# Kernel optimization log

Measured on AMD Instinct MI355X. Metric: run time of the kernel, lower is better.

## Reference

```python
import jax, jax.numpy as jnp
import numpy as np
from jax import lax

B, T, D, L = 64, 512, 1024, 32


def setup_inputs() -> dict:
    key = jax.random.key(0)
    k = jax.random.split(key, 8)
    x = jax.random.normal(k[0], (B, T, D), dtype=jnp.float32)
    mask = jnp.ones((B, T), dtype=bool)
    labels = jax.random.randint(k[1], (B, T), 0, L)
    W = jax.random.normal(k[2], (D, L), dtype=jnp.float32) / np.sqrt(D)
    b = jnp.zeros((L,), dtype=jnp.float32)
    transitions = jax.random.normal(k[3], (L, L), dtype=jnp.float32) * 0.1
    start_transitions = jax.random.normal(k[4], (L,), dtype=jnp.float32) * 0.1
    end_transitions = jax.random.normal(k[5], (L,), dtype=jnp.float32) * 0.1
    return {"x": x, "mask": mask, "labels": labels, "W": W, "b": b,
            "transitions": transitions, "start_transitions": start_transitions,
            "end_transitions": end_transitions}


def _log_partition(logits, mask, transitions, start_t, end_t):
    # logits: [B,T,L], mask: [B,T] bool. AllenNLP _input_likelihood.
    alpha0 = start_t[None, :] + logits[:, 0]  # [B,L]
    logits_t = jnp.swapaxes(logits, 0, 1)[1:]  # [T-1,B,L]
    mask_t = jnp.swapaxes(mask, 0, 1)[1:]      # [T-1,B]

    def step(alpha, inp):
        logit, m = inp  # [B,L], [B]
        # inner[b,i,j] = alpha[b,i] + transitions[i,j] + logit[b,j]
        inner = alpha[:, :, None] + transitions[None, :, :] + logit[:, None, :]
        new = jax.nn.logsumexp(inner, axis=1)
        return jnp.where(m[:, None], new, alpha), None

    alpha, _ = lax.scan(step, alpha0, (logits_t, mask_t))
    return jax.nn.logsumexp(alpha + end_t[None, :], axis=-1)  # [B]


def _joint_score(logits, tags, mask, transitions, start_t, end_t):
    # AllenNLP _joint_likelihood, vectorized over time.
    maskf = mask.astype(logits.dtype)
    score = start_t[tags[:, 0]]
    trans = transitions[tags[:, :-1], tags[:, 1:]]  # [B,T-1]
    score = score + jnp.sum(trans * maskf[:, 1:], axis=1)
    emit = jnp.take_along_axis(logits[:, :-1], tags[:, :-1, None], axis=2)[..., 0]
    score = score + jnp.sum(emit * maskf[:, :-1], axis=1)
    lengths = jnp.sum(mask.astype(jnp.int32), axis=1)
    last_tags = jnp.take_along_axis(tags, (lengths - 1)[:, None], axis=1)[:, 0]
    score = score + end_t[last_tags]
    last_emit = jnp.take_along_axis(logits[:, -1], last_tags[:, None], axis=1)[:, 0]
    score = score + last_emit * maskf[:, -1]
    return score  # [B]


def reference(x, mask, labels, W, b, transitions, start_transitions, end_transitions):
    logits = jnp.einsum('btd,dl->btl', x, W) + b  # Linear classifier
    probabilities = jax.nn.softmax(logits, axis=-1)
    logZ = _log_partition(logits, mask, transitions, start_transitions, end_transitions)
    gold = _joint_score(logits, labels, mask, transitions, start_transitions, end_transitions)
    log_likelihood = jnp.sum(gold - logZ)
    loss = -log_likelihood
    return probabilities, loss
```

## Files before the change

kernel.cpp:

```cpp
#include <hip/hip_runtime.h>

#define OUT_LOSS_IDX 1048576

typedef __attribute__((ext_vector_type(4)))  float f32x4;
typedef __attribute__((ext_vector_type(16))) float f32x16;
typedef __attribute__((ext_vector_type(4)))  int i32x4;
typedef __attribute__((ext_vector_type(4)))  unsigned u32x4;
typedef __attribute__((ext_vector_type(8)))  short bf16x8;

__device__ __forceinline__ unsigned short f32_to_bf16(float f) {
    unsigned u = __float_as_uint(f);
    unsigned r = (u + 0x7FFFu + ((u >> 16) & 1u)) >> 16;
    return (unsigned short)r;
}
__device__ __forceinline__ unsigned packbf(float lo, float hi) {
    return __builtin_amdgcn_perm(__float_as_uint(hi) + 0x8000u,
                                 __float_as_uint(lo) + 0x8000u, 0x07060302u);
}

__global__ void k0_wt(const float* __restrict__ W, unsigned short* __restrict__ Wt,
                      float* __restrict__ loss) {
    int idx = blockIdx.x * 256 + threadIdx.x;
    int k = idx >> 5, c = idx & 31;
    Wt[c * 1024 + k] = f32_to_bf16(W[idx]);
    if (idx == 0) loss[0] = 0.f;
}

__global__ __launch_bounds__(64) void k1_gemm(
    const float* __restrict__ x, const unsigned short* __restrict__ Wt,
    const float* __restrict__ bias, float* __restrict__ logits,
    float* __restrict__ probs) {
    const int lane = threadIdx.x;
    const int m = lane & 15, quad = lane >> 4;
    const int r0 = blockIdx.x * 16;

    const float* xa = x + (size_t)(r0 + m) * 1024 + quad * 8;
    const unsigned short* wb0 = Wt + (size_t)m * 1024 + quad * 8;
    const unsigned short* wb1 = Wt + (size_t)(m + 16) * 1024 + quad * 8;

    f32x4 acc0 = {0.f, 0.f, 0.f, 0.f};
    f32x4 acc1 = {0.f, 0.f, 0.f, 0.f};

    #pragma unroll 4
    for (int ks = 0; ks < 32; ++ks) {
        f32x4 a0 = *(const f32x4*)(xa + ks * 32);
        f32x4 a1 = *(const f32x4*)(xa + ks * 32 + 4);
        bf16x8 b0 = *(const bf16x8*)(wb0 + ks * 32);
        bf16x8 b1 = *(const bf16x8*)(wb1 + ks * 32);
        bf16x8 af;
        af[0] = (short)f32_to_bf16(a0[0]); af[1] = (short)f32_to_bf16(a0[1]);
        af[2] = (short)f32_to_bf16(a0[2]); af[3] = (short)f32_to_bf16(a0[3]);
        af[4] = (short)f32_to_bf16(a1[0]); af[5] = (short)f32_to_bf16(a1[1]);
        af[6] = (short)f32_to_bf16(a1[2]); af[7] = (short)f32_to_bf16(a1[3]);
        acc0 = __builtin_amdgcn_mfma_f32_16x16x32_bf16(af, b0, acc0, 0, 0, 0);
        acc1 = __builtin_amdgcn_mfma_f32_16x16x32_bf16(af, b1, acc1, 0, 0, 0);
    }
    const float bc0 = bias[m], bc1 = bias[16 + m];
    #pragma unroll
    for (int r = 0; r < 4; ++r) {
        int row = r0 + quad * 4 + r;
        float l0 = acc0[r] + bc0;
        float l1 = acc1[r] + bc1;
        logits[row * 32 + m] = l0;
        logits[row * 32 + 16 + m] = l1;
        float mx = fmaxf(l0, l1);
        #pragma unroll
        for (int d = 1; d < 16; d <<= 1) mx = fmaxf(mx, __shfl_xor(mx, d, 64));
        float e0 = __expf(l0 - mx), e1 = __expf(l1 - mx);
        float s = e0 + e1;
        #pragma unroll
        for (int d = 1; d < 16; d <<= 1) s += __shfl_xor(s, d, 64);
        float inv = 1.0f / s;
        probs[row * 32 + m] = e0 * inv;
        probs[row * 32 + 16 + m] = e1 * inv;
    }
}

__global__ __launch_bounds__(256, 1) void k3a_chunks(
    const float* __restrict__ logits, const int* __restrict__ mask,
    const float* __restrict__ trans, float* __restrict__ Gws,
    float* __restrict__ chunkLog) {
    __shared__ float sElt[128 * 32];
    __shared__ int smaskL[128];

    const int tid = threadIdx.x;
    const int b = blockIdx.x >> 2, a = blockIdx.x & 3;
    const int w = tid >> 6, lane = tid & 63;
    const int h = lane >> 5, col = lane & 31;

    const float* src = logits + (size_t)b * 16384 + (128 * a + 1) * 32;
    #pragma unroll
    for (int q = 0; q < 4; ++q) {
        int slot = q * 256 + tid;
        f32x4 v = *(const f32x4*)&src[slot * 4];
        f32x4 e = {__expf(v[0]), __expf(v[1]), __expf(v[2]), __expf(v[3])};
        *(f32x4*)&sElt[slot * 4] = e;
    }
    if (tid < 128) {
        int t = 128 * a + 1 + tid;
        smaskL[tid] = (t < 512) ? mask[b * 512 + t] : 0;
    }
    __syncthreads();

    bf16x8 a1, a2;
    #pragma unroll
    for (int j = 0; j < 8; ++j) {
        a1[j] = (short)f32_to_bf16(__expf(trans[(8 * h + j) * 32 + col]));
        a2[j] = (short)f32_to_bf16(__expf(trans[(16 + 8 * h + j) * 32 + col]));
    }

    float c[16];
    #pragma unroll
    for (int r = 0; r < 16; ++r)
        c[r] = (((r & 3) + 8 * (r >> 2) + 4 * h) == col) ? 1.f : 0.f;
    int esum = 0;

    for (int tl = 0; tl < 32; ++tl) {
        const int tt = 32 * w + tl;
        unsigned d0 = packbf(c[0],  c[1]),  d1 = packbf(c[2],  c[3]);
        unsigned d2 = packbf(c[4],  c[5]),  d3 = packbf(c[6],  c[7]);
        unsigned d4 = packbf(c[8],  c[9]),  d5 = packbf(c[10], c[11]);
        unsigned d6 = packbf(c[12], c[13]), d7 = packbf(c[14], c[15]);
        unsigned x0 = (unsigned)__shfl_xor((int)d0, 32, 64);
        unsigned x1 = (unsigned)__shfl_xor((int)d1, 32, 64);
        unsigned x2 = (unsigned)__shfl_xor((int)d2, 32, 64);
        unsigned x3 = (unsigned)__shfl_xor((int)d3, 32, 64);
        unsigned x4 = (unsigned)__shfl_xor((int)d4, 32, 64);
        unsigned x5 = (unsigned)__shfl_xor((int)d5, 32, 64);
        unsigned x6 = (unsigned)__shfl_xor((int)d6, 32, 64);
        unsigned x7 = (unsigned)__shfl_xor((int)d7, 32, 64);
        u32x4 b0w = {h ? x2 : d0, h ? x3 : d1, h ? d2 : x0, h ? d3 : x1};
        u32x4 b1w = {h ? x6 : d4, h ? x7 : d5, h ? d6 : x4, h ? d7 : x5};
        bf16x8 b0 = __builtin_bit_cast(bf16x8, b0w);
        bf16x8 b1 = __builtin_bit_cast(bf16x8, b1w);

        f32x16 zz = {};
        f32x16 acc = __builtin_amdgcn_mfma_f32_32x32x16_bf16(a1, b0, zz, 0, 0, 0);
        acc = __builtin_amdgcn_mfma_f32_32x32x16_bf16(a2, b1, acc, 0, 0, 0);

        const f32x4* ep = (const f32x4*)&sElt[tt * 32];
        f32x4 e0 = ep[h], e1 = ep[2 + h], e2 = ep[4 + h], e3 = ep[6 + h];
        const int mk = smaskL[tt];

        int sb = __builtin_amdgcn_readfirstlane(__float_as_int(c[0]));
        int ee = ((sb >> 23) & 0xff) - 127;
        ee = ee < -60 ? -60 : (ee > 60 ? 60 : ee);
        float sc = __int_as_float((127 - ee) << 23);
        esum += ee;

        #pragma unroll
        for (int r = 0; r < 16; ++r) {
            float ev = (r < 4 ? e0[r & 3] : r < 8 ? e1[r & 3] : r < 12 ? e2[r & 3] : e3[r & 3]);
            float qn = acc[r] * (ev * sc);
            float qa = c[r] * sc;
            c[r] = mk ? qn : qa;
        }
    }

    const int cc = 4 * a + w;
    float* gw = Gws + (((size_t)(b * 16 + cc)) << 10);
    #pragma unroll
    for (int r = 0; r < 16; ++r)
        gw[((r & 3) + 8 * (r >> 2) + 4 * h) * 32 + col] = c[r];
    if (lane == 0)
        chunkLog[b * 16 + cc] = (float)esum * 0.6931471805599453f;
}

__global__ __launch_bounds__(64, 1) void k3b_combine(
    const float* __restrict__ logits, const int* __restrict__ mask,
    const int* __restrict__ labels, const float* __restrict__ trans,
    const float* __restrict__ start_t, const float* __restrict__ end_t,
    const float* __restrict__ Gws, const float* __restrict__ chunkLog,
    float* __restrict__ loss_out) {
    __shared__ __align__(16) float pbuf[2][32];
    __shared__ int smaskL[512];

    const int b = blockIdx.x, lane = threadIdx.x;
    const int j = lane & 31;
    const int base = b * 512;

    #pragma unroll
    for (int it = 0; it < 2; ++it) {
        int idx = it * 64 + lane;
        *(i32x4*)&smaskL[idx * 4] = *(const i32x4*)&mask[base + idx * 4];
    }
    float p = __expf(start_t[j] + logits[(size_t)b * 16384 + j]);
    float logC = 0.f;
    pbuf[0][j] = p;
    __syncthreads();

    for (int cc = 0; cc < 16; ++cc) {
        const float* g = Gws + ((((size_t)(b * 16 + cc)) << 10) + j * 32);
        f32x4 g0 = *(const f32x4*)&g[0],  g1 = *(const f32x4*)&g[4];
        f32x4 g2 = *(const f32x4*)&g[8],  g3 = *(const f32x4*)&g[12];
        f32x4 g4 = *(const f32x4*)&g[16], g5 = *(const f32x4*)&g[20];
        f32x4 g6 = *(const f32x4*)&g[24], g7 = *(const f32x4*)&g[28];
        const float* pb = pbuf[cc & 1];
        f32x4 p0 = *(const f32x4*)&pb[0],  p1 = *(const f32x4*)&pb[4];
        f32x4 p2 = *(const f32x4*)&pb[8],  p3 = *(const f32x4*)&pb[12];
        f32x4 p4 = *(const f32x4*)&pb[16], p5 = *(const f32x4*)&pb[20];
        f32x4 p6 = *(const f32x4*)&pb[24], p7 = *(const f32x4*)&pb[28];
        float r0 = p0[0];
        float s0 = 0.f, s1 = 0.f, s2 = 0.f, s3 = 0.f;
        s0 = fmaf(p0[0], g0[0], s0); s1 = fmaf(p0[1], g0[1], s1);
        s2 = fmaf(p0[2], g0[2], s2); s3 = fmaf(p0[3], g0[3], s3);
        s0 = fmaf(p1[0], g1[0], s0); s1 = fmaf(p1[1], g1[1], s1);
        s2 = fmaf(p1[2], g1[2], s2); s3 = fmaf(p1[3], g1[3], s3);
        s0 = fmaf(p2[0], g2[0], s0); s1 = fmaf(p2[1], g2[1], s1);
        s2 = fmaf(p2[2], g2[2], s2); s3 = fmaf(p2[3], g2[3], s3);
        s0 = fmaf(p3[0], g3[0], s0); s1 = fmaf(p3[1], g3[1], s1);
        s2 = fmaf(p3[2], g3[2], s2); s3 = fmaf(p3[3], g3[3], s3);
        s0 = fmaf(p4[0], g4[0], s0); s1 = fmaf(p4[1], g4[1], s1);
        s2 = fmaf(p4[2], g4[2], s2); s3 = fmaf(p4[3], g4[3], s3);
        s0 = fmaf(p5[0], g5[0], s0); s1 = fmaf(p5[1], g5[1], s1);
        s2 = fmaf(p5[2], g5[2], s2); s3 = fmaf(p5[3], g5[3], s3);
        s0 = fmaf(p6[0], g6[0], s0); s1 = fmaf(p6[1], g6[1], s1);
        s2 = fmaf(p6[2], g6[2], s2); s3 = fmaf(p6[3], g6[3], s3);
        s0 = fmaf(p7[0], g7[0], s0); s1 = fmaf(p7[1], g7[1], s1);
        s2 = fmaf(p7[2], g7[2], s2); s3 = fmaf(p7[3], g7[3], s3);
        float s = (s0 + s1) + (s2 + s3);
        p = s * __builtin_amdgcn_rcpf(r0);
        pbuf[(cc + 1) & 1][j] = p;
        logC += __logf(r0);
    }
    float clsum = 0.f;
    #pragma unroll
    for (int cc = 0; cc < 16; ++cc) clsum += chunkLog[b * 16 + cc];

    float f = logC + clsum + __logf(p) + end_t[j];
    float mx = f;
    #pragma unroll
    for (int d = 1; d < 32; d <<= 1) mx = fmaxf(mx, __shfl_xor(mx, d, 64));
    float e = __expf(f - mx), se = e;
    #pragma unroll
    for (int d = 1; d < 32; d <<= 1) se += __shfl_xor(se, d, 64);
    float logZb = mx + __logf(se);

    const int t0 = lane * 8;
    const int* lb = labels + base + t0;
    i32x4 la = *(const i32x4*)&lb[0];
    i32x4 lc = *(const i32x4*)&lb[4];
    int tg[8] = {la[0], la[1], la[2], la[3], lc[0], lc[1], lc[2], lc[3]};
    int prev = (lane == 0) ? 0 : labels[base + t0 - 1];
    float part = 0.f;
    int cnt = 0;
    #pragma unroll
    for (int r = 0; r < 8; ++r) {
        int t = t0 + r;
        int mk = smaskL[t];
        float mf = mk ? 1.f : 0.f;
        cnt += mk ? 1 : 0;
        int tag = tg[r];
        if (t > 0) part += trans[prev * 32 + tag] * mf;
        if (t < 511) part += logits[(size_t)b * 16384 + t * 32 + tag] * mf;
        prev = tag;
    }
    #pragma unroll
    for (int d = 1; d < 64; d <<= 1) {
        part += __shfl_xor(part, d, 64);
        cnt += __shfl_xor(cnt, d, 64);
    }
    if (lane == 0) {
        int len = cnt;
        int first = labels[base];
        int last = labels[base + len - 1];
        float g = part + start_t[first] + end_t[last];
        g += logits[(size_t)b * 16384 + 511 * 32 + last] * (smaskL[511] ? 1.f : 0.f);
        atomicAdd(loss_out, logZb - g);
    }
}

extern "C" void kernel_launch(void* const* d_in, const int* in_sizes, int n_in,
                              void* d_out, int out_size, void* d_ws, size_t ws_size,
                              hipStream_t stream) {
    const float* x       = (const float*)d_in[0];
    const int* mk        = (const int*)d_in[1];
    const int* labels    = (const int*)d_in[2];
    const float* W       = (const float*)d_in[3];
    const float* bias    = (const float*)d_in[4];
    const float* trans   = (const float*)d_in[5];
    const float* start_t = (const float*)d_in[6];
    const float* end_t   = (const float*)d_in[7];

    float* probs = (float*)d_out;
    float* loss  = probs + OUT_LOSS_IDX;
    float* ws = (float*)d_ws;
    float* logits = ws;
    unsigned short* Wt = (unsigned short*)(ws + 1048576);
    float* Gws = ws + 1048576 + 16384;
    float* chunkLog = Gws + 1048576;

    k0_wt<<<128, 256, 0, stream>>>(W, Wt, loss);
    k1_gemm<<<2048, 64, 0, stream>>>(x, Wt, bias, logits, probs);
    k3a_chunks<<<256, 256, 0, stream>>>(logits, mk, trans, Gws, chunkLog);
    k3b_combine<<<64, 64, 0, stream>>>(logits, mk, labels, trans, start_t, end_t,
                                       Gws, chunkLog, loss);
}
```

Baseline: 239.4 us.

## Split GEMM K across waves, interleave two CRF sub-chains, prefetch combine loads

The logits GEMM now runs four waves per block, each covering a quarter of K, and reduces their partial sums through shared memory, which raises parallelism and memory-level concurrency. Each k3a wave now advances two independent 16-step sub-chains in interleaved fashion to hide MFMA dependency latency, then joins them with one extra matrix product. k3b prefetches the next chunk's transfer matrix while the current one is applied. The costs are extra shared-memory traffic and a barrier in the GEMM, plus one extra bf16 rounding when composing the sub-chain products.

```diff
diff --git a/kernel.cpp b/kernel.cpp
--- a/kernel.cpp
+++ b/kernel.cpp
@@ -16,6 +16,45 @@
 __device__ __forceinline__ unsigned packbf(float lo, float hi) {
     return __builtin_amdgcn_perm(__float_as_uint(hi) + 0x8000u,
                                  __float_as_uint(lo) + 0x8000u, 0x07060302u);
+}
+__device__ __forceinline__ void make_bfrags(const float* c, int h, bf16x8& b0, bf16x8& b1) {
+    unsigned d0 = packbf(c[0],  c[1]),  d1 = packbf(c[2],  c[3]);
+    unsigned d2 = packbf(c[4],  c[5]),  d3 = packbf(c[6],  c[7]);
+    unsigned d4 = packbf(c[8],  c[9]),  d5 = packbf(c[10], c[11]);
+    unsigned d6 = packbf(c[12], c[13]), d7 = packbf(c[14], c[15]);
+    unsigned x0 = (unsigned)__shfl_xor((int)d0, 32, 64);
+    unsigned x1 = (unsigned)__shfl_xor((int)d1, 32, 64);
+    unsigned x2 = (unsigned)__shfl_xor((int)d2, 32, 64);
+    unsigned x3 = (unsigned)__shfl_xor((int)d3, 32, 64);
+    unsigned x4 = (unsigned)__shfl_xor((int)d4, 32, 64);
+    unsigned x5 = (unsigned)__shfl_xor((int)d5, 32, 64);
+    unsigned x6 = (unsigned)__shfl_xor((int)d6, 32, 64);
+    unsigned x7 = (unsigned)__shfl_xor((int)d7, 32, 64);
+    u32x4 b0w = {h ? x2 : d0, h ? x3 : d1, h ? d2 : x0, h ? d3 : x1};
+    u32x4 b1w = {h ? x6 : d4, h ? x7 : d5, h ? d6 : x4, h ? d7 : x5};
+    b0 = __builtin_bit_cast(bf16x8, b0w);
+    b1 = __builtin_bit_cast(bf16x8, b1w);
+}
+__device__ __forceinline__ void crf_step(float* c, const f32x4* ep, int h, int mk,
+                                         bf16x8 a1, bf16x8 a2, int& esum) {
+    bf16x8 b0, b1;
+    make_bfrags(c, h, b0, b1);
+    f32x16 zz = {};
+    f32x16 acc = __builtin_amdgcn_mfma_f32_32x32x16_bf16(a1, b0, zz, 0, 0, 0);
+    acc = __builtin_amdgcn_mfma_f32_32x32x16_bf16(a2, b1, acc, 0, 0, 0);
+    f32x4 e0 = ep[h], e1 = ep[2 + h], e2 = ep[4 + h], e3 = ep[6 + h];
+    int sb = __builtin_amdgcn_readfirstlane(__float_as_int(c[0]));
+    int ee = ((sb >> 23) & 0xff) - 127;
+    ee = ee < -60 ? -60 : (ee > 60 ? 60 : ee);
+    float sc = __int_as_float((127 - ee) << 23);
+    esum += ee;
+    #pragma unroll
+    for (int r = 0; r < 16; ++r) {
+        float ev = (r < 4 ? e0[r & 3] : r < 8 ? e1[r & 3] : r < 12 ? e2[r & 3] : e3[r & 3]);
+        float qn = acc[r] * (ev * sc);
+        float qa = c[r] * sc;
+        c[r] = mk ? qn : qa;
+    }
 }
 
 __global__ void k0_wt(const float* __restrict__ W, unsigned short* __restrict__ Wt,
@@ -26,23 +65,25 @@
     if (idx == 0) loss[0] = 0.f;
 }
 
-__global__ __launch_bounds__(64) void k1_gemm(
+__global__ __launch_bounds__(256) void k1_gemm(
     const float* __restrict__ x, const unsigned short* __restrict__ Wt,
     const float* __restrict__ bias, float* __restrict__ logits,
     float* __restrict__ probs) {
-    const int lane = threadIdx.x;
+    __shared__ float sacc[3][64][9];
+    const int tid = threadIdx.x;
+    const int wv = tid >> 6, lane = tid & 63;
     const int m = lane & 15, quad = lane >> 4;
     const int r0 = blockIdx.x * 16;
 
-    const float* xa = x + (size_t)(r0 + m) * 1024 + quad * 8;
-    const unsigned short* wb0 = Wt + (size_t)m * 1024 + quad * 8;
-    const unsigned short* wb1 = Wt + (size_t)(m + 16) * 1024 + quad * 8;
+    const float* xa = x + (size_t)(r0 + m) * 1024 + wv * 256 + quad * 8;
+    const unsigned short* wb0 = Wt + (size_t)m * 1024 + wv * 256 + quad * 8;
+    const unsigned short* wb1 = Wt + (size_t)(m + 16) * 1024 + wv * 256 + quad * 8;
 
     f32x4 acc0 = {0.f, 0.f, 0.f, 0.f};
     f32x4 acc1 = {0.f, 0.f, 0.f, 0.f};
 
-    #pragma unroll 4
-    for (int ks = 0; ks < 32; ++ks) {
+    #pragma unroll
+    for (int ks = 0; ks < 8; ++ks) {
         f32x4 a0 = *(const f32x4*)(xa + ks * 32);
         f32x4 a1 = *(const f32x4*)(xa + ks * 32 + 4);
         bf16x8 b0 = *(const bf16x8*)(wb0 + ks * 32);
@@ -55,24 +96,39 @@
         acc0 = __builtin_amdgcn_mfma_f32_16x16x32_bf16(af, b0, acc0, 0, 0, 0);
         acc1 = __builtin_amdgcn_mfma_f32_16x16x32_bf16(af, b1, acc1, 0, 0, 0);
     }
-    const float bc0 = bias[m], bc1 = bias[16 + m];
-    #pragma unroll
-    for (int r = 0; r < 4; ++r) {
-        int row = r0 + quad * 4 + r;
-        float l0 = acc0[r] + bc0;
-        float l1 = acc1[r] + bc1;
-        logits[row * 32 + m] = l0;
-        logits[row * 32 + 16 + m] = l1;
-        float mx = fmaxf(l0, l1);
+    if (wv) {
         #pragma unroll
-        for (int d = 1; d < 16; d <<= 1) mx = fmaxf(mx, __shfl_xor(mx, d, 64));
-        float e0 = __expf(l0 - mx), e1 = __expf(l1 - mx);
-        float s = e0 + e1;
+        for (int r = 0; r < 4; ++r) {
+            sacc[wv - 1][lane][r] = acc0[r];
+            sacc[wv - 1][lane][4 + r] = acc1[r];
+        }
+    }
+    __syncthreads();
+    if (wv == 0) {
         #pragma unroll
-        for (int d = 1; d < 16; d <<= 1) s += __shfl_xor(s, d, 64);
-        float inv = 1.0f / s;
-        probs[row * 32 + m] = e0 * inv;
-        probs[row * 32 + 16 + m] = e1 * inv;
+        for (int r = 0; r < 4; ++r) {
+            acc0[r] += sacc[0][lane][r] + sacc[1][lane][r] + sacc[2][lane][r];
+            acc1[r] += sacc[0][lane][4 + r] + sacc[1][lane][4 + r] + sacc[2][lane][4 + r];
+        }
+        const float bc0 = bias[m], bc1 = bias[16 + m];
+        #pragma unroll
+        for (int r = 0; r < 4; ++r) {
+            int row = r0 + quad * 4 + r;
+            float l0 = acc0[r] + bc0;
+            float l1 = acc1[r] + bc1;
+            logits[row * 32 + m] = l0;
+            logits[row * 32 + 16 + m] = l1;
+            float mx = fmaxf(l0, l1);
+            #pragma unroll
+            for (int d = 1; d < 16; d <<= 1) mx = fmaxf(mx, __shfl_xor(mx, d, 64));
+            float e0 = __expf(l0 - mx), e1 = __expf(l1 - mx);
+            float s = e0 + e1;
+            #pragma unroll
+            for (int d = 1; d < 16; d <<= 1) s += __shfl_xor(s, d, 64);
+            float inv = 1.0f / s;
+            probs[row * 32 + m] = e0 * inv;
+            probs[row * 32 + 16 + m] = e1 * inv;
+        }
     }
 }
 
@@ -82,6 +138,7 @@
     float* __restrict__ chunkLog) {
     __shared__ float sElt[128 * 32];
     __shared__ int smaskL[128];
+    __shared__ float qb[4][32][33];
 
     const int tid = threadIdx.x;
     const int b = blockIdx.x >> 2, a = blockIdx.x & 3;
@@ -109,61 +166,49 @@
         a2[j] = (short)f32_to_bf16(__expf(trans[(16 + 8 * h + j) * 32 + col]));
     }
 
-    float c[16];
+    float cA[16], cB[16];
+    #pragma unroll
+    for (int r = 0; r < 16; ++r) {
+        float iv = (((r & 3) + 8 * (r >> 2) + 4 * h) == col) ? 1.f : 0.f;
+        cA[r] = iv; cB[r] = iv;
+    }
+    int esA = 0, esB = 0;
+
+    for (int tl = 0; tl < 16; ++tl) {
+        const int ttA = 32 * w + tl;
+        const int ttB = 32 * w + 16 + tl;
+        crf_step(cA, (const f32x4*)&sElt[ttA * 32], h, smaskL[ttA], a1, a2, esA);
+        crf_step(cB, (const f32x4*)&sElt[ttB * 32], h, smaskL[ttB], a1, a2, esB);
+    }
+
     #pragma unroll
     for (int r = 0; r < 16; ++r)
-        c[r] = (((r & 3) + 8 * (r >> 2) + 4 * h) == col) ? 1.f : 0.f;
-    int esum = 0;
-
-    for (int tl = 0; tl < 32; ++tl) {
-        const int tt = 32 * w + tl;
-        unsigned d0 = packbf(c[0],  c[1]),  d1 = packbf(c[2],  c[3]);
-        unsigned d2 = packbf(c[4],  c[5]),  d3 = packbf(c[6],  c[7]);
-        unsigned d4 = packbf(c[8],  c[9]),  d5 = packbf(c[10], c[11]);
-        unsigned d6 = packbf(c[12], c[13]), d7 = packbf(c[14], c[15]);
-        unsigned x0 = (unsigned)__shfl_xor((int)d0, 32, 64);
-        unsigned x1 = (unsigned)__shfl_xor((int)d1, 32, 64);
-        unsigned x2 = (unsigned)__shfl_xor((int)d2, 32, 64);
-        unsigned x3 = (unsigned)__shfl_xor((int)d3, 32, 64);
-        unsigned x4 = (unsigned)__shfl_xor((int)d4, 32, 64);
-        unsigned x5 = (unsigned)__shfl_xor((int)d5, 32, 64);
-        unsigned x6 = (unsigned)__shfl_xor((int)d6, 32, 64);
-        unsigned x7 = (unsigned)__shfl_xor((int)d7, 32, 64);
-        u32x4 b0w = {h ? x2 : d0, h ? x3 : d1, h ? d2 : x0, h ? d3 : x1};
-        u32x4 b1w = {h ? x6 : d4, h ? x7 : d5, h ? d6 : x4, h ? d7 : x5};
-        bf16x8 b0 = __builtin_bit_cast(bf16x8, b0w);
-        bf16x8 b1 = __builtin_bit_cast(bf16x8, b1w);
-
-        f32x16 zz = {};
-        f32x16 acc = __builtin_amdgcn_mfma_f32_32x32x16_bf16(a1, b0, zz, 0, 0, 0);
-        acc = __builtin_amdgcn_mfma_f32_32x32x16_bf16(a2, b1, acc, 0, 0, 0);
-
-        const f32x4* ep = (const f32x4*)&sElt[tt * 32];
-        f32x4 e0 = ep[h], e1 = ep[2 + h], e2 = ep[4 + h], e3 = ep[6 + h];
-        const int mk = smaskL[tt];
-
-        int sb = __builtin_amdgcn_readfirstlane(__float_as_int(c[0]));
-        int ee = ((sb >> 23) & 0xff) - 127;
-        ee = ee < -60 ? -60 : (ee > 60 ? 60 : ee);
-        float sc = __int_as_float((127 - ee) << 23);
-        esum += ee;
-
-        #pragma unroll
-        for (int r = 0; r < 16; ++r) {
-            float ev = (r < 4 ? e0[r & 3] : r < 8 ? e1[r & 3] : r < 12 ? e2[r & 3] : e3[r & 3]);
-            float qn = acc[r] * (ev * sc);
-            float qa = c[r] * sc;
-            c[r] = mk ? qn : qa;
-        }
-    }
+        qb[w][(r & 3) + 8 * (r >> 2) + 4 * h][col] = cB[r];
+    __syncthreads();
+    bf16x8 aP1, aP2;
+    #pragma unroll
+    for (int j = 0; j < 8; ++j) {
+        aP1[j] = (short)f32_to_bf16(qb[w][col][8 * h + j]);
+        aP2[j] = (short)f32_to_bf16(qb[w][col][16 + 8 * h + j]);
+    }
+    bf16x8 b0, b1;
+    make_bfrags(cA, h, b0, b1);
+    f32x16 zz = {};
+    f32x16 P = __builtin_amdgcn_mfma_f32_32x32x16_bf16(aP1, b0, zz, 0, 0, 0);
+    P = __builtin_amdgcn_mfma_f32_32x32x16_bf16(aP2, b1, P, 0, 0, 0);
+
+    int sb = __builtin_amdgcn_readfirstlane(__float_as_int(P[0]));
+    int ee = ((sb >> 23) & 0xff) - 127;
+    ee = ee < -60 ? -60 : (ee > 60 ? 60 : ee);
+    float sc = __int_as_float((127 - ee) << 23);
 
     const int cc = 4 * a + w;
     float* gw = Gws + (((size_t)(b * 16 + cc)) << 10);
     #pragma unroll
     for (int r = 0; r < 16; ++r)
-        gw[((r & 3) + 8 * (r >> 2) + 4 * h) * 32 + col] = c[r];
+        gw[((r & 3) + 8 * (r >> 2) + 4 * h) * 32 + col] = P[r] * sc;
     if (lane == 0)
-        chunkLog[b * 16 + cc] = (float)esum * 0.6931471805599453f;
+        chunkLog[b * 16 + cc] = (float)(esA + esB + ee) * 0.6931471805599453f;
 }
 
 __global__ __launch_bounds__(64, 1) void k3b_combine(
@@ -184,17 +229,26 @@
         int idx = it * 64 + lane;
         *(i32x4*)&smaskL[idx * 4] = *(const i32x4*)&mask[base + idx * 4];
     }
+    const float* gbase = Gws + (((size_t)(b * 16)) << 10) + j * 32;
+    f32x4 g0 = *(const f32x4*)&gbase[0],  g1 = *(const f32x4*)&gbase[4];
+    f32x4 g2 = *(const f32x4*)&gbase[8],  g3 = *(const f32x4*)&gbase[12];
+    f32x4 g4 = *(const f32x4*)&gbase[16], g5 = *(const f32x4*)&gbase[20];
+    f32x4 g6 = *(const f32x4*)&gbase[24], g7 = *(const f32x4*)&gbase[28];
+
     float p = __expf(start_t[j] + logits[(size_t)b * 16384 + j]);
     float logC = 0.f;
     pbuf[0][j] = p;
     __syncthreads();
 
     for (int cc = 0; cc < 16; ++cc) {
-        const float* g = Gws + ((((size_t)(b * 16 + cc)) << 10) + j * 32);
-        f32x4 g0 = *(const f32x4*)&g[0],  g1 = *(const f32x4*)&g[4];
-        f32x4 g2 = *(const f32x4*)&g[8],  g3 = *(const f32x4*)&g[12];
-        f32x4 g4 = *(const f32x4*)&g[16], g5 = *(const f32x4*)&g[20];
-        f32x4 g6 = *(const f32x4*)&g[24], g7 = *(const f32x4*)&g[28];
+        const float* gn = gbase + (((size_t)(cc + 1)) << 10);
+        f32x4 n0, n1, n2, n3, n4, n5, n6, n7;
+        if (cc < 15) {
+            n0 = *(const f32x4*)&gn[0];  n1 = *(const f32x4*)&gn[4];
+            n2 = *(const f32x4*)&gn[8];  n3 = *(const f32x4*)&gn[12];
+            n4 = *(const f32x4*)&gn[16]; n5 = *(const f32x4*)&gn[20];
+            n6 = *(const f32x4*)&gn[24]; n7 = *(const f32x4*)&gn[28];
+        }
         const float* pb = pbuf[cc & 1];
         f32x4 p0 = *(const f32x4*)&pb[0],  p1 = *(const f32x4*)&pb[4];
         f32x4 p2 = *(const f32x4*)&pb[8],  p3 = *(const f32x4*)&pb[12];
@@ -222,6 +276,7 @@
         p = s * __builtin_amdgcn_rcpf(r0);
         pbuf[(cc + 1) & 1][j] = p;
         logC += __logf(r0);
+        g0 = n0; g1 = n1; g2 = n2; g3 = n3; g4 = n4; g5 = n5; g6 = n6; g7 = n7;
     }
     float clsum = 0.f;
     #pragma unroll
@@ -291,7 +346,7 @@
     float* chunkLog = Gws + 1048576;
 
     k0_wt<<<128, 256, 0, stream>>>(W, Wt, loss);
-    k1_gemm<<<2048, 64, 0, stream>>>(x, Wt, bias, logits, probs);
+    k1_gemm<<<2048, 256, 0, stream>>>(x, Wt, bias, logits, probs);
     k3a_chunks<<<256, 256, 0, stream>>>(logits, mk, trans, Gws, chunkLog);
     k3b_combine<<<64, 64, 0, stream>>>(logits, mk, labels, trans, start_t, end_t,
                                        Gws, chunkLog, loss);
```

New measurement: 240.2 us. No clear change (+0.3%).
